# Optimization experiments

Hardware: AMD Instinct MI355X
Metric: run time of the kernel (lower is better)

## Reference

```python
import jax, jax.numpy as jnp
import numpy as np

EPS = 1e-5
N_HEADS = 8
CLAMP = 100.0


def layernorm(x, g, b):
    m = x.mean(-1, keepdims=True)
    v = x.var(-1, keepdims=True)  # biased var, matches torch LayerNorm
    return (x - m) / jnp.sqrt(v + EPS) * g + b


def depthwise7(x, w, b):
    # x: [B,C,H,W], w: [C,1,7,7] depthwise (groups=C), pad=3
    y = jax.lax.conv_general_dilated(
        x, w, window_strides=(1, 1), padding=[(3, 3), (3, 3)],
        dimension_numbers=('NCHW', 'OIHW', 'NCHW'),
        feature_group_count=x.shape[1])
    return y + b[None, :, None, None]


def setup_inputs() -> dict:
    key = jax.random.key(0)
    ks = jax.random.split(key, 12)
    B, N, C = 8, 4096, 512
    KH = 7
    s = 0.02
    return {
        'x': jax.random.normal(ks[0], (B, N, C), jnp.float32),
        'qkv_w': jax.random.normal(ks[1], (C, 3 * C), jnp.float32) * s,
        'qkv_b': jnp.zeros((3 * C,), jnp.float32),
        'out_w': jax.random.normal(ks[2], (C, C), jnp.float32) * s,
        'out_b': jnp.zeros((C,), jnp.float32),
        'pre_g': jnp.ones((C,), jnp.float32),
        'pre_b': jnp.zeros((C,), jnp.float32),
        'lcm_g': jnp.ones((C,), jnp.float32),
        'lcm_b': jnp.zeros((C,), jnp.float32),
        'ci_w': jax.random.normal(ks[3], (C, 1, KH, KH), jnp.float32) * s,
        'ci_b': jnp.zeros((C,), jnp.float32),
        'bn_g': jnp.ones((C,), jnp.float32),
        'bn_b': jnp.zeros((C,), jnp.float32),
        'co_w': jax.random.normal(ks[4], (C, 1, KH, KH), jnp.float32) * s,
        'co_b': jnp.zeros((C,), jnp.float32),
        'H': 64,
        'W': 64,
    }


def reference(x, qkv_w, qkv_b, out_w, out_b, pre_g, pre_b, lcm_g, lcm_b,
              ci_w, ci_b, bn_g, bn_b, co_w, co_b, H, W):
    B, N, C = x.shape
    hd = C // N_HEADS
    normed = layernorm(x, pre_g, pre_b)
    qkv = normed @ qkv_w + qkv_b                       # [B,N,3C]
    qkv = qkv.reshape(B, N, 3, N_HEADS, hd).transpose(2, 0, 3, 1, 4)
    q = jax.nn.relu(qkv[0])                            # [B,h,N,d]
    k = jax.nn.relu(qkv[1])
    v = qkv[2]
    kv = jnp.einsum('bhnd,bhnv->bhdv', k, v)           # O(N d^2) associativity trick
    normalizer = jnp.maximum(k.sum(2, keepdims=True), CLAMP)  # [B,h,1,d]
    attn = jnp.einsum('bhnd,bhdv->bhnv', q, kv)
    denom = jnp.maximum((q * normalizer).sum(-1, keepdims=True), CLAMP)
    attn = attn / denom
    attn = attn.transpose(0, 2, 1, 3).reshape(B, N, C)
    attn = attn @ out_w + out_b
    # Local Concentration Module on lcm_norm(attn)
    t = layernorm(attn, lcm_g, lcm_b)
    xi = t.transpose(0, 2, 1).reshape(B, C, H, W)
    y = depthwise7(xi, ci_w, ci_b)
    y = jax.nn.gelu(y, approximate=False)
    m = y.mean((0, 2, 3), keepdims=True)               # BatchNorm2d training-mode stats
    var = y.var((0, 2, 3), keepdims=True)
    y = (y - m) / jnp.sqrt(var + EPS) * bn_g[None, :, None, None] + bn_b[None, :, None, None]
    y = depthwise7(y, co_w, co_b)
    lcm_out = y.reshape(B, C, N).transpose(0, 2, 1)
    return x + attn + lcm_out
```

## Files before the change

### kernel.cpp

```cpp
#include <hip/hip_runtime.h>
#include <math.h>

typedef short v8s __attribute__((ext_vector_type(8)));
typedef short v4s __attribute__((ext_vector_type(4)));
typedef float v4f __attribute__((ext_vector_type(4)));

__device__ __forceinline__ float b2f(unsigned short u) {
    return __uint_as_float(((unsigned)u) << 16);
}
__device__ __forceinline__ unsigned short f2b(float f) {
    unsigned u = __float_as_uint(f);
    unsigned r = (u + 0x7FFF + ((u >> 16) & 1)) >> 16;
    return (unsigned short)r;
}

__device__ __forceinline__ void gl_lds16(const unsigned short* g, unsigned short* l) {
    __builtin_amdgcn_global_load_lds(
        (const __attribute__((address_space(1))) void*)g,
        (__attribute__((address_space(3))) void*)l,
        16, 0, 0);
}

__global__ __launch_bounds__(256) void zero_fill(float* __restrict__ p, int n) {
    int i = blockIdx.x * 256 + threadIdx.x;
    if (i < n) p[i] = 0.0f;
}

__global__ __launch_bounds__(256) void ln_apply(const float* __restrict__ x,
                                                const float* __restrict__ g,
                                                const float* __restrict__ bt,
                                                unsigned short* __restrict__ out) {
    size_t row = blockIdx.x;
    const float2* p = (const float2*)(x + row * 512);
    int t = threadIdx.x;
    float2 v = p[t];
    float s = v.x + v.y, s2 = v.x * v.x + v.y * v.y;
    for (int o = 32; o > 0; o >>= 1) {
        s += __shfl_down(s, o);
        s2 += __shfl_down(s2, o);
    }
    __shared__ float rs[4], rq[4];
    int wave = t >> 6, lane = t & 63;
    if (lane == 0) { rs[wave] = s; rq[wave] = s2; }
    __syncthreads();
    float ts = rs[0] + rs[1] + rs[2] + rs[3];
    float tq = rq[0] + rq[1] + rq[2] + rq[3];
    float mean = ts * (1.0f / 512.0f);
    float var = tq * (1.0f / 512.0f) - mean * mean;
    float inv = rsqrtf(var + 1e-5f);
    float2 gg = ((const float2*)g)[t];
    float2 bb = ((const float2*)bt)[t];
    ushort2 o2;
    o2.x = f2b((v.x - mean) * inv * gg.x + bb.x);
    o2.y = f2b((v.y - mean) * inv * gg.y + bb.y);
    *(ushort2*)&out[row * 512 + 2 * t] = o2;
}

__global__ __launch_bounds__(256) void transpose_f2b(const float* __restrict__ in,
                                                     unsigned short* __restrict__ out,
                                                     int R, int C) {
    __shared__ unsigned short tile[32][33];
    int c0 = blockIdx.x * 32, r0 = blockIdx.y * 32;
    int tx = threadIdx.x, ty = threadIdx.y;
    for (int j = 0; j < 32; j += 8)
        tile[ty + j][tx] = f2b(in[(size_t)(r0 + ty + j) * C + c0 + tx]);
    __syncthreads();
    for (int j = 0; j < 32; j += 8)
        out[(size_t)(c0 + ty + j) * R + r0 + tx] = tile[tx][ty + j];
}

template <int NB, bool QKV>
__global__ __launch_bounds__(512, 4) void gemm256(const unsigned short* __restrict__ A,
                                                  const unsigned short* __restrict__ Bt,
                                                  const float* __restrict__ bias,
                                                  unsigned short* __restrict__ o0,
                                                  unsigned short* __restrict__ o1,
                                                  unsigned short* __restrict__ o2) {
    __shared__ __align__(16) unsigned short LB[3][12288];
    int t = threadIdx.x;
    int wave = t >> 6, lane = t & 63;
    int wm = wave >> 1, wn = wave & 1;
    int mrow = lane & 15, kq4 = lane >> 4;
    int nwg = gridDim.x;
    int cpx = nwg >> 3;
    int bid = blockIdx.x;
    int swz = (bid & 7) * cpx + (bid >> 3);
    int n0 = (swz % NB) * 128;
    int m0 = (swz / NB) * 256;
    const unsigned short* Ab = A + (size_t)m0 * 512;
    const unsigned short* Bb = Bt + (size_t)n0 * 512;
    int rA0 = t >> 2;
    int cA0 = (((t & 3) ^ ((rA0 >> 1) & 3)) * 8);
    int rA1 = 128 + (t >> 2);
    int cA1 = (((t & 3) ^ ((rA1 >> 1) & 3)) * 8);
    size_t srcA0 = (size_t)rA0 * 512 + cA0;
    size_t srcA1 = (size_t)rA1 * 512 + cA1;
    unsigned offA0 = wave * 512;
    unsigned offA1 = 4096 + wave * 512;
    unsigned offB  = 8192 + wave * 512;
    v4f acc[4][4] = {};
    int swr = ((kq4 ^ ((mrow >> 1) & 3)) * 8);

#define STAGE(kt, slot)                                          \
    do {                                                         \
        const unsigned short* aS = Ab + (size_t)(kt) * 32;       \
        const unsigned short* bS = Bb + (size_t)(kt) * 32;       \
        gl_lds16(aS + srcA0, &LB[slot][offA0]);                  \
        gl_lds16(aS + srcA1, &LB[slot][offA1]);                  \
        gl_lds16(bS + srcA0, &LB[slot][offB]);                   \
    } while (0)

    STAGE(0, 0);
    STAGE(1, 1);
    for (int kt = 0; kt < 16; ++kt) {
        if (kt < 15) {
            asm volatile("s_waitcnt vmcnt(3)" ::: "memory");
        } else {
            asm volatile("s_waitcnt vmcnt(0)" ::: "memory");
        }
        __builtin_amdgcn_s_barrier();
        asm volatile("" ::: "memory");
        if (kt + 2 < 16) STAGE(kt + 2, (kt + 2) % 3);
        const unsigned short* as = LB[kt % 3];
        const unsigned short* bs = LB[kt % 3] + 8192;
        v8s af[4], bf[4];
#pragma unroll
        for (int i = 0; i < 4; i++)
            af[i] = *(const v8s*)&as[(wm * 64 + i * 16 + mrow) * 32 + swr];
#pragma unroll
        for (int j = 0; j < 4; j++)
            bf[j] = *(const v8s*)&bs[(wn * 64 + j * 16 + mrow) * 32 + swr];
        __builtin_amdgcn_s_setprio(1);
#pragma unroll
        for (int i = 0; i < 4; i++)
#pragma unroll
            for (int j = 0; j < 4; j++)
                acc[i][j] = __builtin_amdgcn_mfma_f32_16x16x32_bf16(af[i], bf[j], acc[i][j], 0, 0, 0);
        __builtin_amdgcn_s_setprio(0);
    }
#undef STAGE
    __syncthreads();
    unsigned short* CT = &LB[0][0];
    bool doRelu = QKV && (n0 < 1024);
#pragma unroll
    for (int j = 0; j < 4; j++) {
        int col = wn * 64 + j * 16 + mrow;
        float bv = bias[n0 + col];
        int gr = col >> 3;
        int gb = col & 7;
#pragma unroll
        for (int i = 0; i < 4; i++) {
            int rowb = wm * 64 + i * 16 + kq4 * 4;
#pragma unroll
            for (int r = 0; r < 4; r++) {
                int row = rowb + r;
                float v = acc[i][j][r] + bv;
                if (doRelu) v = fmaxf(v, 0.0f);
                CT[row * 128 + ((gr ^ (row & 7)) << 3) + gb] = f2b(v);
            }
        }
    }
    __syncthreads();
    unsigned short* base;
    int cb;
    if (QKV) {
        int seg = n0 >> 9;
        base = (seg == 0) ? o0 : ((seg == 1) ? o1 : o2);
        cb = n0 & 511;
    } else {
        base = o0;
        cb = n0;
    }
#pragma unroll
    for (int p = 0; p < 8; p++) {
        int g = p * 512 + t;
        int row = g >> 4, gl = g & 15;
        int phys = gl ^ (row & 7);
        v8s v = *(const v8s*)&CT[row * 128 + (phys << 3)];
        *(v8s*)&base[(size_t)(m0 + row) * 512 + cb + gl * 8] = v;
    }
}

__global__ __launch_bounds__(256) void kv_part(const unsigned short* __restrict__ kbuf,
                                               const unsigned short* __restrict__ vbuf,
                                               float* __restrict__ kvp,
                                               float* __restrict__ ksp) {
    int bh = blockIdx.x;
    int b = bh >> 3, h = bh & 7;
    int nc = blockIdx.y;
    __shared__ __align__(16) unsigned short kb[64 * 64];
    __shared__ __align__(16) unsigned short vb[64 * 64];
    int t = threadIdx.x;
    int dk0 = (t >> 4) * 4;
    int dv0 = (t & 15) * 4;
    float acc[4][4] = {};
    float ks[4] = {};
    int lr = t >> 2, lc = (t & 3) * 16;
    for (int n0 = nc * 128; n0 < nc * 128 + 128; n0 += 64) {
        __syncthreads();
        size_t base = ((size_t)(b * 4096 + n0 + lr)) * 512 + h * 64;
        *(v8s*)&kb[lr * 64 + lc]     = *(const v8s*)&kbuf[base + lc];
        *(v8s*)&kb[lr * 64 + lc + 8] = *(const v8s*)&kbuf[base + lc + 8];
        *(v8s*)&vb[lr * 64 + lc]     = *(const v8s*)&vbuf[base + lc];
        *(v8s*)&vb[lr * 64 + lc + 8] = *(const v8s*)&vbuf[base + lc + 8];
        __syncthreads();
#pragma unroll 4
        for (int nn = 0; nn < 64; nn++) {
            v4s kr = *(const v4s*)&kb[nn * 64 + dk0];
            v4s vr = *(const v4s*)&vb[nn * 64 + dv0];
            float kf[4], vf[4];
#pragma unroll
            for (int i = 0; i < 4; i++) { kf[i] = b2f((unsigned short)kr[i]); vf[i] = b2f((unsigned short)vr[i]); }
#pragma unroll
            for (int i = 0; i < 4; i++) {
#pragma unroll
                for (int j = 0; j < 4; j++) acc[i][j] += kf[i] * vf[j];
            }
            if ((t & 15) == 0) {
#pragma unroll
                for (int i = 0; i < 4; i++) ks[i] += kf[i];
            }
        }
    }
    float* dst = kvp + ((size_t)(bh * 32 + nc)) * 4096;
#pragma unroll
    for (int i = 0; i < 4; i++)
        *(float4*)&dst[(dk0 + i) * 64 + dv0] = make_float4(acc[i][0], acc[i][1], acc[i][2], acc[i][3]);
    if ((t & 15) == 0) {
        float* kd = ksp + ((size_t)(bh * 32 + nc)) * 64;
#pragma unroll
        for (int i = 0; i < 4; i++) kd[dk0 + i] = ks[i];
    }
}

__global__ __launch_bounds__(256) void kv_reduce(const float* __restrict__ kvp,
                                                 const float* __restrict__ ksp,
                                                 float* __restrict__ kvb,
                                                 float* __restrict__ ksum) {
    int tid = blockIdx.x * 256 + threadIdx.x;
    int bh = tid >> 12, e = tid & 4095;
    float s = 0.0f;
#pragma unroll 8
    for (int c = 0; c < 32; c++) s += kvp[((size_t)(bh * 32 + c)) * 4096 + e];
    kvb[(size_t)bh * 4096 + e] = s;
    if (tid < 4096) {
        int bh2 = tid >> 6, dk = tid & 63;
        float t = 0.0f;
#pragma unroll 8
        for (int c = 0; c < 32; c++) t += ksp[((size_t)(bh2 * 32 + c)) * 64 + dk];
        ksum[tid] = t;
    }
}

__global__ __launch_bounds__(256) void attn_kernel(unsigned short* qa,
                                                   const float* __restrict__ kv,
                                                   const float* __restrict__ ksum) {
    int bh = blockIdx.y;
    int b = bh >> 3, h = bh & 7;
    int nt = blockIdx.x;
    __shared__ float kvs[64 * 64];
    __shared__ float nrm[64];
    int t = threadIdx.x;
    for (int i = t; i < 4096; i += 256) kvs[i] = kv[(size_t)bh * 4096 + i];
    if (t < 64) nrm[t] = fmaxf(ksum[bh * 64 + t], 100.0f);
    __syncthreads();
    int n = nt * 256 + t;
    unsigned short* qp = qa + ((size_t)(b * 4096 + n)) * 512 + h * 64;
    float qf[64];
#pragma unroll
    for (int i = 0; i < 64; i += 8) {
        v8s v = *(const v8s*)&qp[i];
#pragma unroll
        for (int j = 0; j < 8; j++) qf[i + j] = b2f((unsigned short)v[j]);
    }
    float denom = 0.0f;
#pragma unroll
    for (int d = 0; d < 64; d++) denom += qf[d] * nrm[d];
    denom = fmaxf(denom, 100.0f);
    float inv = 1.0f / denom;
#pragma unroll
    for (int dv = 0; dv < 64; dv += 16) {
        float o[16] = {};
        for (int dk = 0; dk < 64; dk++) {
            float q = qf[dk];
#pragma unroll
            for (int i = 0; i < 16; i++) o[i] += q * kvs[dk * 64 + dv + i];
        }
        v8s ov0, ov1;
#pragma unroll
        for (int i = 0; i < 8; i++) {
            ov0[i] = (short)f2b(o[i] * inv);
            ov1[i] = (short)f2b(o[i + 8] * inv);
        }
        *(v8s*)&qp[dv] = ov0;
        *(v8s*)&qp[dv + 8] = ov1;
    }
}

__global__ __launch_bounds__(256) void ln2_transpose(const unsigned short* __restrict__ in,
                                                     const float* __restrict__ g,
                                                     const float* __restrict__ bt,
                                                     unsigned short* __restrict__ out) {
    int bid = blockIdx.x;
    int b = bid >> 6;
    int n0 = (bid & 63) * 64;
    __shared__ float gs[512], bs[512];
    __shared__ __align__(16) unsigned short tile[512 * 64];
    int t = threadIdx.x;
    for (int i = t; i < 512; i += 256) { gs[i] = g[i]; bs[i] = bt[i]; }
    int nl = t >> 2, sub = t & 3;
    const unsigned short* src = in + ((size_t)(b * 4096 + n0 + nl)) * 512 + sub * 8;
    v8s vv[16];
#pragma unroll
    for (int c16 = 0; c16 < 16; c16++)
        vv[c16] = *(const v8s*)&src[c16 * 32];
    float s = 0.f, s2 = 0.f;
#pragma unroll
    for (int c16 = 0; c16 < 16; c16++)
#pragma unroll
        for (int j = 0; j < 8; j++) {
            float f = b2f((unsigned short)vv[c16][j]);
            s += f; s2 += f * f;
        }
    s += __shfl_xor(s, 1); s2 += __shfl_xor(s2, 1);
    s += __shfl_xor(s, 2); s2 += __shfl_xor(s2, 2);
    float mean = s * (1.f / 512.f);
    float var = s2 * (1.f / 512.f) - mean * mean;
    float inv = rsqrtf(var + 1e-5f);
    __syncthreads();
#pragma unroll
    for (int c16 = 0; c16 < 16; c16++) {
        int cb_ = sub * 8 + c16 * 32;
#pragma unroll
        for (int j = 0; j < 8; j++) {
            int c = cb_ + j;
            float f = b2f((unsigned short)vv[c16][j]);
            float y = (f - mean) * inv * gs[c] + bs[c];
            tile[c * 64 + ((((nl >> 3) ^ (c & 7)) << 3) | (nl & 7))] = f2b(y);
        }
    }
    __syncthreads();
    unsigned short* dst = out + ((size_t)b * 512) * 4096 + n0;
#pragma unroll
    for (int p = 0; p < 16; p++) {
        int chunk = p * 256 + t;
        int c = chunk >> 3, gseg = chunk & 7;
        int phys = gseg ^ (c & 7);
        v8s v = *(const v8s*)&tile[c * 64 + phys * 8];
        *(v8s*)&dst[(size_t)c * 4096 + gseg * 8] = v;
    }
}

__global__ __launch_bounds__(256) void dwconv7_gelu(const unsigned short* __restrict__ in,
                                                    const float* __restrict__ w,
                                                    const float* __restrict__ bias,
                                                    unsigned short* __restrict__ out,
                                                    float* __restrict__ bn_sum,
                                                    float* __restrict__ bn_sumsq) {
    int bc = blockIdx.x;
    int c = bc & 511;
    __shared__ float img[70 * 72];
    __shared__ float wsm[49];
    __shared__ float r1[4], r2[4];
    int t = threadIdx.x;
    int tx = t & 63, ty = t >> 6;
    for (int i = t; i < 70 * 72; i += 256) img[i] = 0.0f;
    if (t < 49) wsm[t] = w[c * 49 + t];
    __syncthreads();
    const unsigned short* src = in + (size_t)bc * 4096;
#pragma unroll
    for (int q = t; q < 512; q += 256) {
        v8s v = *(const v8s*)&src[q * 8];
        float* ip = &img[((q >> 3) + 3) * 72 + (q & 7) * 8 + 3];
#pragma unroll
        for (int j = 0; j < 8; j++) ip[j] = b2f((unsigned short)v[j]);
    }
    __syncthreads();
    float wt[49];
#pragma unroll
    for (int i = 0; i < 49; i++) wt[i] = wsm[i];
    float bv = bias[c];
    float acc[16];
#pragma unroll
    for (int i = 0; i < 16; i++) acc[i] = bv;
    int h0 = ty * 16;
#pragma unroll
    for (int rr = 0; rr < 22; rr++) {
        float v[7];
#pragma unroll
        for (int kw = 0; kw < 7; kw++) v[kw] = img[(h0 + rr) * 72 + tx + kw];
#pragma unroll
        for (int kh = 0; kh < 7; kh++) {
            int o = rr - kh;
            if (o >= 0 && o <= 15) {
                float dot = v[0] * wt[kh * 7];
#pragma unroll
                for (int kw = 1; kw < 7; kw++) dot += v[kw] * wt[kh * 7 + kw];
                acc[o] += dot;
            }
        }
    }
    float s = 0.0f, s2 = 0.0f;
    unsigned short* dst = out + (size_t)bc * 4096;
#pragma unroll
    for (int i = 0; i < 16; i++) {
        float a = acc[i];
        float ge = 0.5f * a * (1.0f + erff(a * 0.70710678118f));
        dst[(h0 + i) * 64 + tx] = f2b(ge);
        s += ge;
        s2 += ge * ge;
    }
    for (int o = 32; o > 0; o >>= 1) {
        s += __shfl_down(s, o);
        s2 += __shfl_down(s2, o);
    }
    int lane = t & 63;
    if (lane == 0) { r1[ty] = s; r2[ty] = s2; }
    __syncthreads();
    if (t == 0) {
        atomicAdd(&bn_sum[c], r1[0] + r1[1] + r1[2] + r1[3]);
        atomicAdd(&bn_sumsq[c], r2[0] + r2[1] + r2[2] + r2[3]);
    }
}

__global__ void bn_finalize(const float* __restrict__ s, const float* __restrict__ s2,
                            const float* __restrict__ g, const float* __restrict__ b,
                            float2* __restrict__ ab) {
    int c = blockIdx.x * blockDim.x + threadIdx.x;
    if (c >= 512) return;
    float m = s[c] * (1.0f / 32768.0f);
    float var = s2[c] * (1.0f / 32768.0f) - m * m;
    float inv = rsqrtf(var + 1e-5f);
    float sc = g[c] * inv;
    ab[c] = make_float2(sc, b[c] - m * sc);
}

__global__ __launch_bounds__(256) void dwconv7_bn(const unsigned short* __restrict__ in,
                                                  const float2* __restrict__ bnab,
                                                  const float* __restrict__ w,
                                                  const float* __restrict__ bias,
                                                  unsigned short* __restrict__ out) {
    int bc = blockIdx.x;
    int c = bc & 511;
    __shared__ float img[70 * 72];
    __shared__ float wsm[49];
    int t = threadIdx.x;
    int tx = t & 63, ty = t >> 6;
    for (int i = t; i < 70 * 72; i += 256) img[i] = 0.0f;
    if (t < 49) wsm[t] = w[c * 49 + t];
    __syncthreads();
    float2 ab = bnab[c];
    const unsigned short* src = in + (size_t)bc * 4096;
#pragma unroll
    for (int q = t; q < 512; q += 256) {
        v8s v = *(const v8s*)&src[q * 8];
        float* ip = &img[((q >> 3) + 3) * 72 + (q & 7) * 8 + 3];
#pragma unroll
        for (int j = 0; j < 8; j++) ip[j] = b2f((unsigned short)v[j]) * ab.x + ab.y;
    }
    __syncthreads();
    float wt[49];
#pragma unroll
    for (int i = 0; i < 49; i++) wt[i] = wsm[i];
    float bv = bias[c];
    float acc[16];
#pragma unroll
    for (int i = 0; i < 16; i++) acc[i] = bv;
    int h0 = ty * 16;
#pragma unroll
    for (int rr = 0; rr < 22; rr++) {
        float v[7];
#pragma unroll
        for (int kw = 0; kw < 7; kw++) v[kw] = img[(h0 + rr) * 72 + tx + kw];
#pragma unroll
        for (int kh = 0; kh < 7; kh++) {
            int o = rr - kh;
            if (o >= 0 && o <= 15) {
                float dot = v[0] * wt[kh * 7];
#pragma unroll
                for (int kw = 1; kw < 7; kw++) dot += v[kw] * wt[kh * 7 + kw];
                acc[o] += dot;
            }
        }
    }
    unsigned short* dst = out + (size_t)bc * 4096;
#pragma unroll
    for (int i = 0; i < 16; i++)
        dst[(h0 + i) * 64 + tx] = f2b(acc[i]);
}

__global__ __launch_bounds__(256) void final_add(const float* __restrict__ x,
                                                 const unsigned short* __restrict__ attn,
                                                 const unsigned short* __restrict__ y2,
                                                 float* __restrict__ out) {
    __shared__ unsigned short tile[32][36];
    int b = blockIdx.z;
    int c0 = blockIdx.x * 32, n0 = blockIdx.y * 32;
    int t = threadIdx.x;
    {
        int c = t >> 3, n4 = (t & 7) * 4;
        ushort4 v = *(const ushort4*)&y2[((size_t)(b * 512 + c0 + c)) * 4096 + n0 + n4];
        tile[c][n4] = v.x; tile[c][n4 + 1] = v.y; tile[c][n4 + 2] = v.z; tile[c][n4 + 3] = v.w;
    }
    __syncthreads();
    int nl = t >> 3, cl = (t & 7) * 4;
    size_t idx = ((size_t)(b * 4096 + n0 + nl)) * 512 + c0 + cl;
    float4 xv = *(const float4*)&x[idx];
    ushort4 av = *(const ushort4*)&attn[idx];
    float4 o;
    o.x = xv.x + b2f(av.x) + b2f(tile[cl][nl]);
    o.y = xv.y + b2f(av.y) + b2f(tile[cl + 1][nl]);
    o.z = xv.z + b2f(av.z) + b2f(tile[cl + 2][nl]);
    o.w = xv.w + b2f(av.w) + b2f(tile[cl + 3][nl]);
    *(float4*)&out[idx] = o;
}

extern "C" void kernel_launch(void* const* d_in, const int* in_sizes, int n_in,
                              void* d_out, int out_size, void* d_ws, size_t ws_size,
                              hipStream_t stream) {
    const float* x     = (const float*)d_in[0];
    const float* qkv_w = (const float*)d_in[1];
    const float* qkv_b = (const float*)d_in[2];
    const float* out_w = (const float*)d_in[3];
    const float* out_b = (const float*)d_in[4];
    const float* pre_g = (const float*)d_in[5];
    const float* pre_b = (const float*)d_in[6];
    const float* lcm_g = (const float*)d_in[7];
    const float* lcm_b = (const float*)d_in[8];
    const float* ci_w  = (const float*)d_in[9];
    const float* ci_b  = (const float*)d_in[10];
    const float* bn_g  = (const float*)d_in[11];
    const float* bn_b  = (const float*)d_in[12];
    const float* co_w  = (const float*)d_in[13];
    const float* co_b  = (const float*)d_in[14];

    char* ws = (char*)d_ws;
    const size_t SLOT = 33554432;
    unsigned short* S0 = (unsigned short*)(ws);
    unsigned short* S1 = (unsigned short*)(ws + SLOT);
    unsigned short* S2 = (unsigned short*)(ws + 2 * SLOT);
    const size_t MISC = 3 * SLOT;
    unsigned short* wT1 = (unsigned short*)(ws + MISC);
    unsigned short* wT2 = (unsigned short*)(ws + MISC + 1572864);
    float* kvb          = (float*)(ws + MISC + 2097152);
    float* ksum         = (float*)(ws + MISC + 2097152 + 1048576);
    float* bn_sum       = (float*)(ws + MISC + 2097152 + 1048576 + 16384);
    float* bn_sumsq     = (float*)(ws + MISC + 2097152 + 1048576 + 16384 + 2048);
    float2* bnab        = (float2*)(ws + MISC + 3166208);
    float* ksp          = (float*)(ws + MISC + 3170304);
    float* outp         = (float*)d_out;

    unsigned short* normed = (unsigned short*)d_out;
    float* kvp             = (float*)((char*)d_out + SLOT);

    dim3 tb(32, 8);
    transpose_f2b<<<dim3(48, 16), tb, 0, stream>>>(qkv_w, wT1, 512, 1536);
    transpose_f2b<<<dim3(16, 16), tb, 0, stream>>>(out_w, wT2, 512, 512);
    zero_fill<<<4, 256, 0, stream>>>(bn_sum, 1024);
    ln_apply<<<32768, 256, 0, stream>>>(x, pre_g, pre_b, normed);
    gemm256<12, true><<<1536, 512, 0, stream>>>(normed, wT1, qkv_b, S0, S1, S2);
    kv_part<<<dim3(64, 32), 256, 0, stream>>>(S1, S2, kvp, ksp);
    kv_reduce<<<1024, 256, 0, stream>>>(kvp, ksp, kvb, ksum);
    attn_kernel<<<dim3(16, 64), 256, 0, stream>>>(S0, kvb, ksum);
    gemm256<4, false><<<512, 512, 0, stream>>>(S0, wT2, out_b, S1, S1, S1);
    ln2_transpose<<<512, 256, 0, stream>>>(S1, lcm_g, lcm_b, S0);
    dwconv7_gelu<<<4096, 256, 0, stream>>>(S0, ci_w, ci_b, S2, bn_sum, bn_sumsq);
    bn_finalize<<<2, 256, 0, stream>>>(bn_sum, bn_sumsq, bn_g, bn_b, bnab);
    dwconv7_bn<<<4096, 256, 0, stream>>>(S2, bnab, co_w, co_b, S0);
    final_add<<<dim3(16, 128, 8), tb.x * tb.y, 0, stream>>>(x, S1, S0, outp);
}
```

Baseline: 518.9 us.

## Move linear-attention KV and output products onto MFMA with transposed K/V layout

```diff
diff --git a/kernel.cpp b/kernel.cpp
--- a/kernel.cpp
+++ b/kernel.cpp
@@ -13,6 +13,7 @@
     unsigned r = (u + 0x7FFF + ((u >> 16) & 1)) >> 16;
     return (unsigned short)r;
 }
+__device__ __forceinline__ int swz8(int row) { return (row & 7) ^ ((row >> 3) & 7); }
 
 __device__ __forceinline__ void gl_lds16(const unsigned short* g, unsigned short* l) {
     __builtin_amdgcn_global_load_lds(
@@ -146,8 +147,7 @@
     for (int j = 0; j < 4; j++) {
         int col = wn * 64 + j * 16 + mrow;
         float bv = bias[n0 + col];
-        int gr = col >> 3;
-        int gb = col & 7;
+        int gr = col >> 3, gb = col & 7;
 #pragma unroll
         for (int i = 0; i < 4; i++) {
             int rowb = wm * 64 + i * 16 + kq4 * 4;
@@ -156,80 +156,122 @@
                 int row = rowb + r;
                 float v = acc[i][j][r] + bv;
                 if (doRelu) v = fmaxf(v, 0.0f);
-                CT[row * 128 + ((gr ^ (row & 7)) << 3) + gb] = f2b(v);
-            }
-        }
-    }
-    __syncthreads();
-    unsigned short* base;
-    int cb;
-    if (QKV) {
-        int seg = n0 >> 9;
-        base = (seg == 0) ? o0 : ((seg == 1) ? o1 : o2);
-        cb = n0 & 511;
+                CT[row * 136 + ((gr ^ swz8(row)) << 3) + gb] = f2b(v);
+            }
+        }
+    }
+    __syncthreads();
+    if (!QKV || n0 < 512) {
+#pragma unroll
+        for (int p = 0; p < 8; p++) {
+            int g = p * 512 + t;
+            int row = g >> 4, gl = g & 15;
+            v8s v = *(const v8s*)&CT[row * 136 + ((gl ^ swz8(row)) << 3)];
+            *(v8s*)&o0[(size_t)(m0 + row) * 512 + n0 + gl * 8] = v;
+        }
     } else {
-        base = o0;
-        cb = n0;
-    }
-#pragma unroll
-    for (int p = 0; p < 8; p++) {
-        int g = p * 512 + t;
-        int row = g >> 4, gl = g & 15;
-        int phys = gl ^ (row & 7);
-        v8s v = *(const v8s*)&CT[row * 128 + (phys << 3)];
-        *(v8s*)&base[(size_t)(m0 + row) * 512 + cb + gl * 8] = v;
-    }
-}
-
-__global__ __launch_bounds__(256) void kv_part(const unsigned short* __restrict__ kbuf,
-                                               const unsigned short* __restrict__ vbuf,
+        unsigned short* Tb = (n0 < 1024) ? o1 : o2;
+        int col = t >> 2, sub = t & 3;
+        int cglob = n0 + col;
+        int hl = (cglob & 511) >> 6, d = cglob & 63;
+        int bb = m0 >> 12, gc = m0 & 4095;
+        unsigned short* dst = Tb + ((size_t)((bb * 8 + hl) * 64 + d)) * 4096 + gc;
+        int cg = col >> 3, cb7 = col & 7;
+#pragma unroll
+        for (int g = 0; g < 8; g++) {
+            v8s v;
+#pragma unroll
+            for (int e = 0; e < 8; e++) {
+                int rr = g * 32 + sub * 8 + e;
+                v[e] = (short)CT[rr * 136 + ((cg ^ swz8(rr)) << 3) + cb7];
+            }
+            *(v8s*)&dst[g * 32 + sub * 8] = v;
+        }
+    }
+}
+
+__global__ __launch_bounds__(256) void kv_part(const unsigned short* __restrict__ kT,
+                                               const unsigned short* __restrict__ vT,
                                                float* __restrict__ kvp,
                                                float* __restrict__ ksp) {
-    int bh = blockIdx.x;
-    int b = bh >> 3, h = bh & 7;
-    int nc = blockIdx.y;
-    __shared__ __align__(16) unsigned short kb[64 * 64];
-    __shared__ __align__(16) unsigned short vb[64 * 64];
-    int t = threadIdx.x;
-    int dk0 = (t >> 4) * 4;
-    int dv0 = (t & 15) * 4;
-    float acc[4][4] = {};
-    float ks[4] = {};
-    int lr = t >> 2, lc = (t & 3) * 16;
-    for (int n0 = nc * 128; n0 < nc * 128 + 128; n0 += 64) {
-        __syncthreads();
-        size_t base = ((size_t)(b * 4096 + n0 + lr)) * 512 + h * 64;
-        *(v8s*)&kb[lr * 64 + lc]     = *(const v8s*)&kbuf[base + lc];
-        *(v8s*)&kb[lr * 64 + lc + 8] = *(const v8s*)&kbuf[base + lc + 8];
-        *(v8s*)&vb[lr * 64 + lc]     = *(const v8s*)&vbuf[base + lc];
-        *(v8s*)&vb[lr * 64 + lc + 8] = *(const v8s*)&vbuf[base + lc + 8];
-        __syncthreads();
-#pragma unroll 4
-        for (int nn = 0; nn < 64; nn++) {
-            v4s kr = *(const v4s*)&kb[nn * 64 + dk0];
-            v4s vr = *(const v4s*)&vb[nn * 64 + dv0];
-            float kf[4], vf[4];
-#pragma unroll
-            for (int i = 0; i < 4; i++) { kf[i] = b2f((unsigned short)kr[i]); vf[i] = b2f((unsigned short)vr[i]); }
-#pragma unroll
-            for (int i = 0; i < 4; i++) {
-#pragma unroll
-                for (int j = 0; j < 4; j++) acc[i][j] += kf[i] * vf[j];
-            }
-            if ((t & 15) == 0) {
-#pragma unroll
-                for (int i = 0; i < 4; i++) ks[i] += kf[i];
-            }
-        }
-    }
-    float* dst = kvp + ((size_t)(bh * 32 + nc)) * 4096;
-#pragma unroll
-    for (int i = 0; i < 4; i++)
-        *(float4*)&dst[(dk0 + i) * 64 + dv0] = make_float4(acc[i][0], acc[i][1], acc[i][2], acc[i][3]);
-    if ((t & 15) == 0) {
-        float* kd = ksp + ((size_t)(bh * 32 + nc)) * 64;
-#pragma unroll
-        for (int i = 0; i < 4; i++) kd[dk0 + i] = ks[i];
+    __shared__ __align__(16) unsigned short LB[3][4096];
+    int bh = blockIdx.x, nc = blockIdx.y;
+    int t = threadIdx.x;
+    int w = t >> 6, lane = t & 63;
+    int wdk = w >> 1, wdv = w & 1;
+    int mrow = lane & 15, kq4 = lane >> 4;
+    const unsigned short* Kb = kT + (size_t)bh * 262144 + nc * 512;
+    const unsigned short* Vb = vT + (size_t)bh * 262144 + nc * 512;
+    int rA = t >> 2;
+    int lcA = (t & 3) ^ (rA & 3);
+    size_t srcoff = (size_t)rA * 4096 + lcA * 8;
+    unsigned dstK = w * 512;
+    unsigned dstV = 2048 + w * 512;
+    v4f acc[2][2] = {};
+    v4f accs[2] = {};
+    v8s ones;
+#pragma unroll
+    for (int jj = 0; jj < 8; jj++) ones[jj] = (short)0x3F80;
+
+#define KSTAGE(ks, slot)                                         \
+    do {                                                         \
+        gl_lds16(Kb + (size_t)(ks) * 32 + srcoff, &LB[slot][dstK]); \
+        gl_lds16(Vb + (size_t)(ks) * 32 + srcoff, &LB[slot][dstV]); \
+    } while (0)
+
+    KSTAGE(0, 0);
+    KSTAGE(1, 1);
+    for (int ks = 0; ks < 16; ++ks) {
+        if (ks < 15) {
+            asm volatile("s_waitcnt vmcnt(2)" ::: "memory");
+        } else {
+            asm volatile("s_waitcnt vmcnt(0)" ::: "memory");
+        }
+        __builtin_amdgcn_s_barrier();
+        asm volatile("" ::: "memory");
+        if (ks + 2 < 16) KSTAGE(ks + 2, (ks + 2) % 3);
+        const unsigned short* as = LB[ks % 3];
+        v8s af[2], bf[2];
+#pragma unroll
+        for (int i = 0; i < 2; i++) {
+            int row = wdk * 32 + i * 16 + mrow;
+            af[i] = *(const v8s*)&as[row * 32 + ((kq4 ^ (row & 3)) << 3)];
+        }
+#pragma unroll
+        for (int j = 0; j < 2; j++) {
+            int row = wdv * 32 + j * 16 + mrow;
+            bf[j] = *(const v8s*)&as[2048 + row * 32 + ((kq4 ^ (row & 3)) << 3)];
+        }
+#pragma unroll
+        for (int i = 0; i < 2; i++)
+#pragma unroll
+            for (int j = 0; j < 2; j++)
+                acc[i][j] = __builtin_amdgcn_mfma_f32_16x16x32_bf16(af[i], bf[j], acc[i][j], 0, 0, 0);
+        if (wdv == 0) {
+#pragma unroll
+            for (int i = 0; i < 2; i++)
+                accs[i] = __builtin_amdgcn_mfma_f32_16x16x32_bf16(af[i], ones, accs[i], 0, 0, 0);
+        }
+    }
+#undef KSTAGE
+    float* dst = kvp + ((size_t)(bh * 8 + nc)) * 4096;
+#pragma unroll
+    for (int i = 0; i < 2; i++)
+#pragma unroll
+        for (int j = 0; j < 2; j++)
+#pragma unroll
+            for (int r = 0; r < 4; r++) {
+                int row = wdk * 32 + i * 16 + kq4 * 4 + r;
+                int col = wdv * 32 + j * 16 + mrow;
+                dst[row * 64 + col] = acc[i][j][r];
+            }
+    if (wdv == 0 && mrow == 0) {
+        float* kd = ksp + ((size_t)(bh * 8 + nc)) * 64 + wdk * 32;
+#pragma unroll
+        for (int i = 0; i < 2; i++)
+#pragma unroll
+            for (int r = 0; r < 4; r++)
+                kd[i * 16 + kq4 * 4 + r] = accs[i][r];
     }
 }
 
@@ -240,60 +282,92 @@
     int tid = blockIdx.x * 256 + threadIdx.x;
     int bh = tid >> 12, e = tid & 4095;
     float s = 0.0f;
-#pragma unroll 8
-    for (int c = 0; c < 32; c++) s += kvp[((size_t)(bh * 32 + c)) * 4096 + e];
+#pragma unroll
+    for (int c = 0; c < 8; c++) s += kvp[((size_t)(bh * 8 + c)) * 4096 + e];
     kvb[(size_t)bh * 4096 + e] = s;
     if (tid < 4096) {
         int bh2 = tid >> 6, dk = tid & 63;
-        float t = 0.0f;
-#pragma unroll 8
-        for (int c = 0; c < 32; c++) t += ksp[((size_t)(bh2 * 32 + c)) * 64 + dk];
-        ksum[tid] = t;
-    }
-}
-
-__global__ __launch_bounds__(256) void attn_kernel(unsigned short* qa,
-                                                   const float* __restrict__ kv,
-                                                   const float* __restrict__ ksum) {
+        float x = 0.0f;
+#pragma unroll
+        for (int c = 0; c < 8; c++) x += ksp[(bh2 * 8 + c) * 64 + dk];
+        ksum[tid] = x;
+    }
+}
+
+__global__ __launch_bounds__(256) void attn_mfma(unsigned short* __restrict__ qa,
+                                                 const float* __restrict__ kv,
+                                                 const float* __restrict__ ksum) {
+    __shared__ __align__(16) unsigned short olds[4][4096];
     int bh = blockIdx.y;
     int b = bh >> 3, h = bh & 7;
-    int nt = blockIdx.x;
-    __shared__ float kvs[64 * 64];
-    __shared__ float nrm[64];
-    int t = threadIdx.x;
-    for (int i = t; i < 4096; i += 256) kvs[i] = kv[(size_t)bh * 4096 + i];
-    if (t < 64) nrm[t] = fmaxf(ksum[bh * 64 + t], 100.0f);
-    __syncthreads();
-    int n = nt * 256 + t;
-    unsigned short* qp = qa + ((size_t)(b * 4096 + n)) * 512 + h * 64;
-    float qf[64];
-#pragma unroll
-    for (int i = 0; i < 64; i += 8) {
-        v8s v = *(const v8s*)&qp[i];
-#pragma unroll
-        for (int j = 0; j < 8; j++) qf[i + j] = b2f((unsigned short)v[j]);
-    }
-    float denom = 0.0f;
-#pragma unroll
-    for (int d = 0; d < 64; d++) denom += qf[d] * nrm[d];
-    denom = fmaxf(denom, 100.0f);
-    float inv = 1.0f / denom;
-#pragma unroll
-    for (int dv = 0; dv < 64; dv += 16) {
-        float o[16] = {};
-        for (int dk = 0; dk < 64; dk++) {
-            float q = qf[dk];
-#pragma unroll
-            for (int i = 0; i < 16; i++) o[i] += q * kvs[dk * 64 + dv + i];
-        }
-        v8s ov0, ov1;
-#pragma unroll
-        for (int i = 0; i < 8; i++) {
-            ov0[i] = (short)f2b(o[i] * inv);
-            ov1[i] = (short)f2b(o[i + 8] * inv);
-        }
-        *(v8s*)&qp[dv] = ov0;
-        *(v8s*)&qp[dv + 8] = ov1;
+    int t = threadIdx.x;
+    int w = t >> 6, lane = t & 63;
+    int mrow = lane & 15, kq4 = lane >> 6 ? 0 : lane >> 4;
+    kq4 = lane >> 4;
+    int nb = blockIdx.x * 256 + w * 64;
+    unsigned short* qbase = qa + ((size_t)(b * 4096 + nb)) * 512 + h * 64;
+    const float* kvb = kv + (size_t)bh * 4096;
+    v4f acc[4][4] = {};
+    v4f accd[4] = {};
+#pragma unroll
+    for (int s = 0; s < 2; s++) {
+        v8s af[4];
+#pragma unroll
+        for (int i = 0; i < 4; i++)
+            af[i] = *(const v8s*)&qbase[(size_t)(i * 16 + mrow) * 512 + s * 32 + kq4 * 8];
+        v8s nh, nl;
+#pragma unroll
+        for (int jj = 0; jj < 8; jj++) {
+            float nv = fmaxf(ksum[bh * 64 + s * 32 + kq4 * 8 + jj], 100.0f);
+            unsigned short hb = f2b(nv);
+            nh[jj] = (short)hb;
+            nl[jj] = (short)f2b(nv - b2f(hb));
+        }
+#pragma unroll
+        for (int i = 0; i < 4; i++) {
+            accd[i] = __builtin_amdgcn_mfma_f32_16x16x32_bf16(af[i], nh, accd[i], 0, 0, 0);
+            accd[i] = __builtin_amdgcn_mfma_f32_16x16x32_bf16(af[i], nl, accd[i], 0, 0, 0);
+        }
+#pragma unroll
+        for (int j = 0; j < 4; j++) {
+            v8s kh, kl;
+#pragma unroll
+            for (int jj = 0; jj < 8; jj++) {
+                float kvv = kvb[(size_t)(s * 32 + kq4 * 8 + jj) * 64 + j * 16 + mrow];
+                unsigned short hb = f2b(kvv);
+                kh[jj] = (short)hb;
+                kl[jj] = (short)f2b(kvv - b2f(hb));
+            }
+#pragma unroll
+            for (int i = 0; i < 4; i++) {
+                acc[i][j] = __builtin_amdgcn_mfma_f32_16x16x32_bf16(af[i], kh, acc[i][j], 0, 0, 0);
+                acc[i][j] = __builtin_amdgcn_mfma_f32_16x16x32_bf16(af[i], kl, acc[i][j], 0, 0, 0);
+            }
+        }
+    }
+    unsigned short* ol = olds[w];
+#pragma unroll
+    for (int i = 0; i < 4; i++) {
+        float inv[4];
+#pragma unroll
+        for (int r = 0; r < 4; r++) inv[r] = 1.0f / fmaxf(accd[i][r], 100.0f);
+#pragma unroll
+        for (int j = 0; j < 4; j++) {
+            int dv = j * 16 + mrow;
+#pragma unroll
+            for (int r = 0; r < 4; r++) {
+                int rl = i * 16 + kq4 * 4 + r;
+                ol[rl * 64 + (((dv >> 3) ^ (rl & 7)) << 3) + (dv & 7)] = f2b(acc[i][j][r] * inv[r]);
+            }
+        }
+    }
+    __syncthreads();
+#pragma unroll
+    for (int p = 0; p < 8; p++) {
+        int idx = p * 64 + lane;
+        int row = idx >> 3, gl = idx & 7;
+        v8s v = *(const v8s*)&ol[row * 64 + ((gl ^ (row & 7)) << 3)];
+        *(v8s*)&qbase[(size_t)row * 512 + gl * 8] = v;
     }
 }
 
@@ -559,9 +633,9 @@
     zero_fill<<<4, 256, 0, stream>>>(bn_sum, 1024);
     ln_apply<<<32768, 256, 0, stream>>>(x, pre_g, pre_b, normed);
     gemm256<12, true><<<1536, 512, 0, stream>>>(normed, wT1, qkv_b, S0, S1, S2);
-    kv_part<<<dim3(64, 32), 256, 0, stream>>>(S1, S2, kvp, ksp);
+    kv_part<<<dim3(64, 8), 256, 0, stream>>>(S1, S2, kvp, ksp);
     kv_reduce<<<1024, 256, 0, stream>>>(kvp, ksp, kvb, ksum);
-    attn_kernel<<<dim3(16, 64), 256, 0, stream>>>(S0, kvb, ksum);
+    attn_mfma<<<dim3(16, 64), 256, 0, stream>>>(S0, kvb, ksum);
     gemm256<4, false><<<512, 512, 0, stream>>>(S0, wT2, out_b, S1, S1, S1);
     ln2_transpose<<<512, 256, 0, stream>>>(S1, lcm_g, lcm_b, S0);
     dwconv7_gelu<<<4096, 256, 0, stream>>>(S0, ci_w, ci_b, S2, bn_sum, bn_sumsq);
```

After: 436.5 us. -15.9%, faster.
